# Optimization experiments

Measured on AMD Instinct MI355X. Metric: run time of the kernel, lower is better.

## Reference

```python
import jax, jax.numpy as jnp
import numpy as np

T_LEN, E_LEN, BATCH, DIM = 32, 256, 16, 512  # topic_len, exp_len, batch, input=hidden size
HID = 512


def setup_inputs() -> dict:
    key = jax.random.key(0)
    k1, k2, k3, k4, k5, k6 = jax.random.split(key, 6)
    topic = jax.random.normal(k1, (T_LEN, BATCH, DIM), dtype=jnp.float32)
    exp_output = jax.random.normal(k2, (E_LEN, BATCH, DIM), dtype=jnp.float32)
    seq_mask = jax.random.bernoulli(k3, 0.1, (E_LEN, BATCH))  # True = masked exp position
    # nn.Linear(hidden+input, hidden): weight [HID, HID+DIM], bias [HID]
    lim1 = 1.0 / np.sqrt(HID + DIM)
    W_attn = jax.random.uniform(k4, (HID, HID + DIM), minval=-lim1, maxval=lim1, dtype=jnp.float32)
    b_attn = jax.random.uniform(k5, (HID,), minval=-lim1, maxval=lim1, dtype=jnp.float32)
    # nn.Linear(hidden, 1): weight [1, HID], bias [1]
    lim2 = 1.0 / np.sqrt(HID)
    kv, kb = jax.random.split(k6)
    v_score = jax.random.uniform(kv, (1, HID), minval=-lim2, maxval=lim2, dtype=jnp.float32)
    b_score = jax.random.uniform(kb, (1,), minval=-lim2, maxval=lim2, dtype=jnp.float32)
    return {"topic": topic, "exp_output": exp_output, "seq_mask": seq_mask,
            "W_attn": W_attn, "b_attn": b_attn, "v_score": v_score, "b_score": b_score}


def reference(topic, exp_output, seq_mask, W_attn, b_attn, v_score, b_score):
    # topic: [T, B, D]; exp_output: [E, B, D]; seq_mask: [E, B] bool
    D = topic.shape[2]
    # Split the concat-Linear: cat(topic, exp) @ W.T == topic @ W[:, :D].T + exp @ W[:, D:].T
    proj_t = jnp.einsum('tbd,hd->bth', topic, W_attn[:, :D])        # [B, T, H]
    proj_e = jnp.einsum('ebd,hd->beh', exp_output, W_attn[:, D:])   # [B, E, H]
    feat = jnp.tanh(proj_t[:, :, None, :] + proj_e[:, None, :, :] + b_attn)  # [B, T, E, H]
    energies = jnp.einsum('bteh,h->bte', feat, v_score[0]) + b_score[0]      # [B, T, E]
    # mask exp positions (broadcast over topic dim), as masked_fill(-1e12)
    energies = jnp.where(seq_mask.T[:, None, :], jnp.float32(-1e12), energies)
    attn_s1 = jax.nn.softmax(jnp.swapaxes(energies, 1, 2), axis=2)  # [B, E, T], softmax over topics
    attn_s2 = jax.nn.softmax(energies, axis=2)                      # [B, T, E], softmax over exp
    new_exp = jnp.einsum('bet,btd->bed', attn_s1, jnp.swapaxes(topic, 0, 1))       # [B, E, D]
    new_topic = jnp.einsum('bte,bed->btd', attn_s2, jnp.swapaxes(exp_output, 0, 1))  # [B, T, D]
    return new_topic, new_exp
```

## Files before the change

### kernel.cpp

```cpp
#include <hip/hip_runtime.h>
#include <hip/hip_bf16.h>
#include <cstddef>
#include <cstdint>

#define T_LEN 32
#define E_LEN 256
#define BATCH 16
#define DIM 512
#define HID 512
#define WROW 1024

#define TWO_LOG2E 2.8853900817779268f

typedef __attribute__((ext_vector_type(8))) short bf16x8;
typedef __attribute__((ext_vector_type(4))) float f32x4;

__device__ inline bf16x8 cvt8(float4 a, float4 b) {
    union { bf16x8 v; __hip_bfloat16 h[8]; } u;
    u.h[0] = __float2bfloat16(a.x); u.h[1] = __float2bfloat16(a.y);
    u.h[2] = __float2bfloat16(a.z); u.h[3] = __float2bfloat16(a.w);
    u.h[4] = __float2bfloat16(b.x); u.h[5] = __float2bfloat16(b.y);
    u.h[6] = __float2bfloat16(b.z); u.h[7] = __float2bfloat16(b.w);
    return u.v;
}

#define GPAD 8
#define GLDR (64 + GPAD)

__global__ __launch_bounds__(256) void gemm_fused(
    const float* __restrict__ topic, const float* __restrict__ expo,
    const float* __restrict__ W, const float* __restrict__ battn,
    float* __restrict__ PT, float* __restrict__ PE) {
    __shared__ __hip_bfloat16 As[64 * GLDR];
    __shared__ __hip_bfloat16 Bs[64 * GLDR];
    const int tid = threadIdx.x;
    const int by = blockIdx.y;
    const float* A; const float* Wp; const float* bias; float* C; int m0;
    if (by < 8) { A = topic; Wp = W;       bias = battn;   C = PT; m0 = by * 64; }
    else        { A = expo;  Wp = W + DIM; bias = nullptr; C = PE; m0 = (by - 8) * 64; }
    const int n0 = blockIdx.x * 64;
    const int w = tid >> 6;
    const int lane = tid & 63;
    const int l15 = lane & 15;
    const int g = lane >> 4;
    const int srow = tid >> 2;
    const int sc = tid & 3;

    f32x4 acc[4];
    const f32x4 z = {0.f, 0.f, 0.f, 0.f};
#pragma unroll
    for (int nt = 0; nt < 4; ++nt) acc[nt] = z;

    const float* ga = A + (size_t)(m0 + srow) * 512 + sc * 8;
    const float* gb = Wp + (size_t)(n0 + srow) * WROW + sc * 8;

    for (int kk = 0; kk < 8; ++kk) {
        float4 a0 = *(const float4*)(ga);
        float4 a1 = *(const float4*)(ga + 4);
        float4 a2 = *(const float4*)(ga + 32);
        float4 a3 = *(const float4*)(ga + 36);
        float4 b0 = *(const float4*)(gb);
        float4 b1 = *(const float4*)(gb + 4);
        float4 b2 = *(const float4*)(gb + 32);
        float4 b3 = *(const float4*)(gb + 36);
        ga += 64; gb += 64;
        bf16x8 av0 = cvt8(a0, a1), av1 = cvt8(a2, a3);
        bf16x8 bv0 = cvt8(b0, b1), bv1 = cvt8(b2, b3);
        __syncthreads();
        *(bf16x8*)&As[srow * GLDR + sc * 8] = av0;
        *(bf16x8*)&As[srow * GLDR + sc * 8 + 32] = av1;
        *(bf16x8*)&Bs[srow * GLDR + sc * 8] = bv0;
        *(bf16x8*)&Bs[srow * GLDR + sc * 8 + 32] = bv1;
        __syncthreads();
#pragma unroll
        for (int s = 0; s < 2; ++s) {
            bf16x8 af = *(const bf16x8*)&As[(w * 16 + l15) * GLDR + (s * 4 + g) * 8];
#pragma unroll
            for (int nt = 0; nt < 4; ++nt) {
                bf16x8 bf = *(const bf16x8*)&Bs[(nt * 16 + l15) * GLDR + (s * 4 + g) * 8];
                acc[nt] = __builtin_amdgcn_mfma_f32_16x16x32_bf16(af, bf, acc[nt], 0, 0, 0);
            }
        }
    }
#pragma unroll
    for (int nt = 0; nt < 4; ++nt) {
        int n = n0 + nt * 16 + l15;
        float bv = bias ? bias[n] : 0.f;
#pragma unroll
        for (int r = 0; r < 4; ++r) {
            int m = m0 + w * 16 + g * 4 + r;
            C[(size_t)m * 512 + n] = (acc[nt][r] + bv) * TWO_LOG2E;
        }
    }
}

__global__ __launch_bounds__(256) void energies_k(const float* __restrict__ PT,
                                                  const float* __restrict__ PE,
                                                  const float* __restrict__ v,
                                                  const float* __restrict__ bscore,
                                                  const int* __restrict__ mask,
                                                  float* __restrict__ EN) {
    const int b = blockIdx.x;
    const int tg = blockIdx.y;
    const int ech = blockIdx.z;
    const int lane = threadIdx.x & 63;
    const int w = threadIdx.x >> 6;
    const int h0 = lane * 8;

    float sv[8], spt[4][8];
    float sumv;
    {
        float4 v0 = *(const float4*)(v + h0);
        float4 v1 = *(const float4*)(v + h0 + 4);
        float vr[8] = {v0.x, v0.y, v0.z, v0.w, v1.x, v1.y, v1.z, v1.w};
        float s = 0.f;
#pragma unroll
        for (int j = 0; j < 8; ++j) { sv[j] = -2.f * vr[j]; s += vr[j]; }
#pragma unroll
        for (int off = 32; off; off >>= 1) s += __shfl_xor(s, off);
        sumv = s;
#pragma unroll
        for (int i = 0; i < 4; ++i) {
            const float* p = PT + ((size_t)((tg * 4 + i) * BATCH + b)) * HID + h0;
            float4 p0 = *(const float4*)(p);
            float4 p1 = *(const float4*)(p + 4);
            spt[i][0] = p0.x; spt[i][1] = p0.y; spt[i][2] = p0.z; spt[i][3] = p0.w;
            spt[i][4] = p1.x; spt[i][5] = p1.y; spt[i][6] = p1.z; spt[i][7] = p1.w;
        }
    }
    const int e0 = ech * 16 + w * 4;
    const float bs = bscore[0];
#pragma unroll
    for (int ei = 0; ei < 4; ++ei) {
        const int e = e0 + ei;
        const float* pe = PE + ((size_t)(e * BATCH + b)) * HID + h0;
        float4 p0 = *(const float4*)(pe);
        float4 p1 = *(const float4*)(pe + 4);
        float pr[8] = {p0.x, p0.y, p0.z, p0.w, p1.x, p1.y, p1.z, p1.w};
        float acc[4] = {0.f, 0.f, 0.f, 0.f};
#pragma unroll
        for (int i = 0; i < 4; ++i) {
#pragma unroll
            for (int j = 0; j < 8; ++j) {
                float x = spt[i][j] + pr[j];
                float ex = __builtin_amdgcn_exp2f(x);
                float r = __builtin_amdgcn_rcpf(ex + 1.f);
                acc[i] = fmaf(sv[j], r, acc[i]);
            }
        }
#pragma unroll
        for (int i = 0; i < 4; ++i) {
#pragma unroll
            for (int off = 32; off; off >>= 1) acc[i] += __shfl_xor(acc[i], off);
        }
        if (lane == 0) {
            const int msk = mask[e * BATCH + b];
#pragma unroll
            for (int i = 0; i < 4; ++i) {
                float en = sumv + bs + acc[i];
                if (msk != 0) en = -1e12f;
                EN[((size_t)b * T_LEN + tg * 4 + i) * E_LEN + e] = en;
            }
        }
    }
}

__global__ __launch_bounds__(256) void new_exp_k(const float* __restrict__ EN,
                                                 const float* __restrict__ topic,
                                                 float* __restrict__ out) {
    const int idx = blockIdx.x * 4 + (threadIdx.x >> 6);
    const int b = idx >> 8;
    const int e = idx & 255;
    const int lane = threadIdx.x & 63;
    float x = (lane < T_LEN) ? EN[((size_t)b * T_LEN + lane) * E_LEN + e] : -3e38f;
    float m = x;
#pragma unroll
    for (int off = 16; off; off >>= 1) m = fmaxf(m, __shfl_xor(m, off));
    float p = (lane < T_LEN) ? __expf(x - m) : 0.f;
    float s = p;
#pragma unroll
    for (int off = 16; off; off >>= 1) s += __shfl_xor(s, off);
    float wv = __fdividef(p, s);
    float acc[8] = {};
    for (int t = 0; t < T_LEN; ++t) {
        const float wt = __shfl(wv, t);
        const float* row = topic + ((size_t)t * BATCH + b) * DIM;
#pragma unroll
        for (int j = 0; j < 8; ++j) acc[j] = fmaf(wt, row[lane + 64 * j], acc[j]);
    }
    float* o = out + ((size_t)b * E_LEN + e) * DIM;
#pragma unroll
    for (int j = 0; j < 8; ++j) o[lane + 64 * j] = acc[j];
}

__global__ __launch_bounds__(256) void new_topic_k(const float* __restrict__ EN,
                                                   const float* __restrict__ expo,
                                                   float* __restrict__ out) {
    const int b = blockIdx.x / T_LEN;
    const int t = blockIdx.x % T_LEN;
    const int tid = threadIdx.x;
    __shared__ float wsm[E_LEN];
    __shared__ float wred[4];
    float x = EN[((size_t)b * T_LEN + t) * E_LEN + tid];
    const int lane = tid & 63;
    const int wid = tid >> 6;
    float m = x;
#pragma unroll
    for (int off = 32; off; off >>= 1) m = fmaxf(m, __shfl_xor(m, off));
    if (lane == 0) wred[wid] = m;
    __syncthreads();
    m = fmaxf(fmaxf(wred[0], wred[1]), fmaxf(wred[2], wred[3]));
    float p = __expf(x - m);
    float s = p;
#pragma unroll
    for (int off = 32; off; off >>= 1) s += __shfl_xor(s, off);
    __syncthreads();
    if (lane == 0) wred[wid] = s;
    __syncthreads();
    s = wred[0] + wred[1] + wred[2] + wred[3];
    wsm[tid] = __fdividef(p, s);
    __syncthreads();
    const float2* ex2 = (const float2*)expo;
    float2 acc = {0.f, 0.f};
#pragma unroll 8
    for (int e = 0; e < E_LEN; ++e) {
        float2 rv = ex2[(size_t)(e * BATCH + b) * 256 + tid];
        const float we = wsm[e];
        acc.x = fmaf(we, rv.x, acc.x);
        acc.y = fmaf(we, rv.y, acc.y);
    }
    float2* o = (float2*)(out + ((size_t)b * T_LEN + t) * DIM);
    o[tid] = acc;
}

extern "C" void kernel_launch(void* const* d_in, const int* in_sizes, int n_in,
                              void* d_out, int out_size, void* d_ws, size_t ws_size,
                              hipStream_t stream) {
    const float* topic = (const float*)d_in[0];
    const float* expo  = (const float*)d_in[1];
    const int*   mask  = (const int*)d_in[2];
    const float* W     = (const float*)d_in[3];
    const float* battn = (const float*)d_in[4];
    const float* vsc   = (const float*)d_in[5];
    const float* bsc   = (const float*)d_in[6];
    float* out = (float*)d_out;

    float* PT = (float*)d_ws;
    float* PE = PT + (size_t)T_LEN * BATCH * HID;
    float* EN = PE + (size_t)E_LEN * BATCH * HID;

    gemm_fused<<<dim3(8, 72), 256, 0, stream>>>(topic, expo, W, battn, PT, PE);
    energies_k<<<dim3(BATCH, 8, 16), 256, 0, stream>>>(PT, PE, vsc, bsc, mask, EN);
    new_exp_k<<<BATCH * E_LEN / 4, 256, 0, stream>>>(EN, topic, out + (size_t)BATCH * T_LEN * DIM);
    new_topic_k<<<BATCH * T_LEN, 256, 0, stream>>>(EN, expo, out);
}
```

Measured before the change: 133.0 us.

## Prefetch GEMM tiles into registers and merge the two attention epilogue kernels

The GEMM loop now loads the next k-slice of A and W into registers before the shared-memory store and MFMA of the current slice, so global load latency overlaps with compute. The new_exp and new_topic kernels are merged into one launch of 2048 blocks that branches on block index. This removes one kernel launch and lets both epilogue parts run concurrently. The new_exp path switches to float4 vectorized loads with contiguous per-lane columns. new_topic is split into two halves of DIM per (b,t), which doubles its parallelism but recomputes the softmax twice.

```diff
diff --git a/kernel.cpp b/kernel.cpp
--- a/kernel.cpp
+++ b/kernel.cpp
@@ -54,18 +54,29 @@
     const float* ga = A + (size_t)(m0 + srow) * 512 + sc * 8;
     const float* gb = Wp + (size_t)(n0 + srow) * WROW + sc * 8;
 
+    float4 a0 = *(const float4*)(ga);
+    float4 a1 = *(const float4*)(ga + 4);
+    float4 a2 = *(const float4*)(ga + 32);
+    float4 a3 = *(const float4*)(ga + 36);
+    float4 b0 = *(const float4*)(gb);
+    float4 b1 = *(const float4*)(gb + 4);
+    float4 b2 = *(const float4*)(gb + 32);
+    float4 b3 = *(const float4*)(gb + 36);
+
     for (int kk = 0; kk < 8; ++kk) {
-        float4 a0 = *(const float4*)(ga);
-        float4 a1 = *(const float4*)(ga + 4);
-        float4 a2 = *(const float4*)(ga + 32);
-        float4 a3 = *(const float4*)(ga + 36);
-        float4 b0 = *(const float4*)(gb);
-        float4 b1 = *(const float4*)(gb + 4);
-        float4 b2 = *(const float4*)(gb + 32);
-        float4 b3 = *(const float4*)(gb + 36);
-        ga += 64; gb += 64;
         bf16x8 av0 = cvt8(a0, a1), av1 = cvt8(a2, a3);
         bf16x8 bv0 = cvt8(b0, b1), bv1 = cvt8(b2, b3);
+        if (kk < 7) {
+            ga += 64; gb += 64;
+            a0 = *(const float4*)(ga);
+            a1 = *(const float4*)(ga + 4);
+            a2 = *(const float4*)(ga + 32);
+            a3 = *(const float4*)(ga + 36);
+            b0 = *(const float4*)(gb);
+            b1 = *(const float4*)(gb + 4);
+            b2 = *(const float4*)(gb + 32);
+            b3 = *(const float4*)(gb + 36);
+        }
         __syncthreads();
         *(bf16x8*)&As[srow * GLDR + sc * 8] = av0;
         *(bf16x8*)&As[srow * GLDR + sc * 8 + 32] = av1;
@@ -165,72 +176,76 @@
     }
 }
 
-__global__ __launch_bounds__(256) void new_exp_k(const float* __restrict__ EN,
-                                                 const float* __restrict__ topic,
-                                                 float* __restrict__ out) {
-    const int idx = blockIdx.x * 4 + (threadIdx.x >> 6);
-    const int b = idx >> 8;
-    const int e = idx & 255;
-    const int lane = threadIdx.x & 63;
-    float x = (lane < T_LEN) ? EN[((size_t)b * T_LEN + lane) * E_LEN + e] : -3e38f;
-    float m = x;
-#pragma unroll
-    for (int off = 16; off; off >>= 1) m = fmaxf(m, __shfl_xor(m, off));
-    float p = (lane < T_LEN) ? __expf(x - m) : 0.f;
-    float s = p;
-#pragma unroll
-    for (int off = 16; off; off >>= 1) s += __shfl_xor(s, off);
-    float wv = __fdividef(p, s);
-    float acc[8] = {};
-    for (int t = 0; t < T_LEN; ++t) {
-        const float wt = __shfl(wv, t);
-        const float* row = topic + ((size_t)t * BATCH + b) * DIM;
-#pragma unroll
-        for (int j = 0; j < 8; ++j) acc[j] = fmaf(wt, row[lane + 64 * j], acc[j]);
-    }
-    float* o = out + ((size_t)b * E_LEN + e) * DIM;
-#pragma unroll
-    for (int j = 0; j < 8; ++j) o[lane + 64 * j] = acc[j];
-}
-
-__global__ __launch_bounds__(256) void new_topic_k(const float* __restrict__ EN,
-                                                   const float* __restrict__ expo,
-                                                   float* __restrict__ out) {
-    const int b = blockIdx.x / T_LEN;
-    const int t = blockIdx.x % T_LEN;
+__global__ __launch_bounds__(256) void epilogue_k(const float* __restrict__ EN,
+                                                  const float* __restrict__ topic,
+                                                  const float* __restrict__ expo,
+                                                  float* __restrict__ out) {
     const int tid = threadIdx.x;
-    __shared__ float wsm[E_LEN];
-    __shared__ float wred[4];
-    float x = EN[((size_t)b * T_LEN + t) * E_LEN + tid];
-    const int lane = tid & 63;
-    const int wid = tid >> 6;
-    float m = x;
-#pragma unroll
-    for (int off = 32; off; off >>= 1) m = fmaxf(m, __shfl_xor(m, off));
-    if (lane == 0) wred[wid] = m;
-    __syncthreads();
-    m = fmaxf(fmaxf(wred[0], wred[1]), fmaxf(wred[2], wred[3]));
-    float p = __expf(x - m);
-    float s = p;
-#pragma unroll
-    for (int off = 32; off; off >>= 1) s += __shfl_xor(s, off);
-    __syncthreads();
-    if (lane == 0) wred[wid] = s;
-    __syncthreads();
-    s = wred[0] + wred[1] + wred[2] + wred[3];
-    wsm[tid] = __fdividef(p, s);
-    __syncthreads();
-    const float2* ex2 = (const float2*)expo;
-    float2 acc = {0.f, 0.f};
+    if (blockIdx.x < 1024) {
+        const int idx = blockIdx.x * 4 + (tid >> 6);
+        const int b = idx >> 8;
+        const int e = idx & 255;
+        const int lane = tid & 63;
+        float x = (lane < T_LEN) ? EN[((size_t)b * T_LEN + lane) * E_LEN + e] : -3e38f;
+        float m = x;
+#pragma unroll
+        for (int off = 16; off; off >>= 1) m = fmaxf(m, __shfl_xor(m, off));
+        float p = (lane < T_LEN) ? __expf(x - m) : 0.f;
+        float s = p;
+#pragma unroll
+        for (int off = 16; off; off >>= 1) s += __shfl_xor(s, off);
+        float wv = __fdividef(p, s);
+        float4 acc0 = {0.f, 0.f, 0.f, 0.f};
+        float4 acc1 = {0.f, 0.f, 0.f, 0.f};
+        const int d0 = lane * 8;
+        for (int t = 0; t < T_LEN; ++t) {
+            const float wt = __shfl(wv, t);
+            const float* row = topic + ((size_t)t * BATCH + b) * DIM + d0;
+            float4 r0 = *(const float4*)(row);
+            float4 r1 = *(const float4*)(row + 4);
+            acc0.x = fmaf(wt, r0.x, acc0.x); acc0.y = fmaf(wt, r0.y, acc0.y);
+            acc0.z = fmaf(wt, r0.z, acc0.z); acc0.w = fmaf(wt, r0.w, acc0.w);
+            acc1.x = fmaf(wt, r1.x, acc1.x); acc1.y = fmaf(wt, r1.y, acc1.y);
+            acc1.z = fmaf(wt, r1.z, acc1.z); acc1.w = fmaf(wt, r1.w, acc1.w);
+        }
+        float* o = out + (size_t)BATCH * T_LEN * DIM + ((size_t)b * E_LEN + e) * DIM + d0;
+        *(float4*)(o) = acc0;
+        *(float4*)(o + 4) = acc1;
+    } else {
+        const int q = blockIdx.x - 1024;
+        const int bt = q >> 1;
+        const int half = q & 1;
+        __shared__ float wsm[E_LEN];
+        __shared__ float wred[4];
+        float x = EN[(size_t)bt * E_LEN + tid];
+        const int lane = tid & 63;
+        const int wid = tid >> 6;
+        float m = x;
+#pragma unroll
+        for (int off = 32; off; off >>= 1) m = fmaxf(m, __shfl_xor(m, off));
+        if (lane == 0) wred[wid] = m;
+        __syncthreads();
+        m = fmaxf(fmaxf(wred[0], wred[1]), fmaxf(wred[2], wred[3]));
+        float p = __expf(x - m);
+        float s = p;
+#pragma unroll
+        for (int off = 32; off; off >>= 1) s += __shfl_xor(s, off);
+        __syncthreads();
+        if (lane == 0) wred[wid] = s;
+        __syncthreads();
+        s = wred[0] + wred[1] + wred[2] + wred[3];
+        wsm[tid] = __fdividef(p, s);
+        __syncthreads();
+        const int b = bt >> 5;
+        const float* base = expo + half * 256 + tid;
+        float acc = 0.f;
 #pragma unroll 8
-    for (int e = 0; e < E_LEN; ++e) {
-        float2 rv = ex2[(size_t)(e * BATCH + b) * 256 + tid];
-        const float we = wsm[e];
-        acc.x = fmaf(we, rv.x, acc.x);
-        acc.y = fmaf(we, rv.y, acc.y);
-    }
-    float2* o = (float2*)(out + ((size_t)b * T_LEN + t) * DIM);
-    o[tid] = acc;
+        for (int e = 0; e < E_LEN; ++e) {
+            float rv = base[(size_t)(e * BATCH + b) * DIM];
+            acc = fmaf(wsm[e], rv, acc);
+        }
+        out[(size_t)bt * DIM + half * 256 + tid] = acc;
+    }
 }
 
 extern "C" void kernel_launch(void* const* d_in, const int* in_sizes, int n_in,
@@ -251,6 +266,5 @@
 
     gemm_fused<<<dim3(8, 72), 256, 0, stream>>>(topic, expo, W, battn, PT, PE);
     energies_k<<<dim3(BATCH, 8, 16), 256, 0, stream>>>(PT, PE, vsc, bsc, mask, EN);
-    new_exp_k<<<BATCH * E_LEN / 4, 256, 0, stream>>>(EN, topic, out + (size_t)BATCH * T_LEN * DIM);
-    new_topic_k<<<BATCH * T_LEN, 256, 0, stream>>>(EN, expo, out);
-}
+    epilogue_k<<<2048, 256, 0, stream>>>(EN, topic, expo, out);
+}
```

After: 129.6 us. 2.5% less time.
